# Kernel optimization log

Hardware: AMD Instinct MI355X
Metric: run time of the kernel (lower is better)

The kernel has to match this reference:

```python
import jax, jax.numpy as jnp
import numpy as np

B, U, C, M = 4096, 1024, 5000, 20

def setup_inputs() -> dict:
    key = jax.random.key(0)
    ks = jax.random.split(key, 9)
    inputs = jax.random.randint(ks[0], (B, 1), 0, C).astype(jnp.int32)
    states = 0.1 * jax.random.normal(ks[1], (B, U + 2), dtype=jnp.float32)
    bias_z = jnp.zeros((U,), jnp.float32)
    recurrent_kernel = 0.02 * jax.random.normal(ks[2], (U, 4 * U), dtype=jnp.float32)
    kernel_c = 0.02 * jax.random.normal(ks[3], (C, 4 * U), dtype=jnp.float32)
    bias = jnp.zeros((3 * U,), jnp.float32)
    kernel_d = 0.1 * jax.random.normal(ks[4], (2, 4 * U), dtype=jnp.float32)
    Wgmm_part1 = 0.05 * jax.random.normal(ks[5], (U, 3 * M), dtype=jnp.float32)
    bgmm_part1 = jnp.zeros((3 * M,), jnp.float32)
    return {"inputs": inputs, "states": states, "bias_z": bias_z,
            "recurrent_kernel": recurrent_kernel, "kernel_c": kernel_c,
            "bias": bias, "kernel_d": kernel_d,
            "Wgmm_part1": Wgmm_part1, "bgmm_part1": bgmm_part1}

def exp_safe(x):
    return jnp.clip(jnp.exp(x), 1e-10, 1e10)

def reference(inputs, states, bias_z, recurrent_kernel, kernel_c, bias,
              kernel_d, Wgmm_part1, bgmm_part1):
    u = bias_z.shape[0]
    h_tm1 = states[:, :-2]          # [B, U]
    _d = states[:, -2:]             # [B, 2]
    ch = inputs[:, 0].astype(jnp.int32)
    # one_hot(ch) @ kernel_c is just a row gather
    pre = kernel_c[ch] + _d @ kernel_d              # [B, 4U]
    # z and r gates share the left operand -> fuse into one matmul
    zr = (h_tm1 @ recurrent_kernel[:, :2 * u] + pre[:, :2 * u]
          + jnp.concatenate([bias_z, bias[:u]]))
    z = jax.nn.sigmoid(zr[:, :u])
    r = jax.nn.sigmoid(zr[:, u:])
    hh = jnp.tanh((r * h_tm1) @ recurrent_kernel[:, 2 * u:3 * u]
                  + pre[:, 2 * u:3 * u] + bias[u:2 * u])
    h = z * h_tm1 + (1.0 - z) * hh
    o = jnp.tanh(h @ recurrent_kernel[:, 3 * u:]
                 + pre[:, 3 * u:] + bias[2 * u:])
    gmm = o @ Wgmm_part1 + bgmm_part1               # [B, 3M]
    _pi, mux, muy = jnp.split(gmm, 3, axis=-1)
    e = exp_safe(_pi)
    pi = e / jnp.sum(e, axis=-1, keepdims=True)
    x_pred = jnp.sum(pi * mux, axis=-1, keepdims=True)
    y_pred = jnp.sum(pi * muy, axis=-1, keepdims=True)
    out = jnp.concatenate([o, pi, mux, muy, x_pred, y_pred], axis=-1)
    new_state = jnp.concatenate([h, x_pred, y_pred], axis=-1)
    return out, new_state
```

## Files before the change

### kernel.cpp

```cpp
#include <hip/hip_runtime.h>

typedef __attribute__((ext_vector_type(8))) short     bf16x8;
typedef __attribute__((ext_vector_type(4))) float     f32x4;
typedef __attribute__((ext_vector_type(2))) float     f32x2;
typedef __attribute__((ext_vector_type(4))) unsigned short u16x4;

#define NB 4096
#define NU 1024
#define OUT_STRIDE 1086
#define NS_STRIDE 1026
#define NS_BASE (4096*1086)

__device__ __forceinline__ unsigned short f2bf(float x) {
  unsigned int u = __float_as_uint(x);
  unsigned int r = (u + 0x7FFFu + ((u >> 16) & 1u)) >> 16;
  return (unsigned short)r;
}
__device__ __forceinline__ float sigmoidf(float x) { return 1.f / (1.f + expf(-x)); }

__device__ __forceinline__ void gld_lds16(const void* g, void* l) {
  __builtin_amdgcn_global_load_lds((const __attribute__((address_space(1))) void*)g,
                                   (__attribute__((address_space(3))) void*)l, 16, 0, 0);
}

__global__ __launch_bounds__(256)
void transposeR(const float* __restrict__ R, unsigned short* __restrict__ Bt) {
  __shared__ float t[64][65];
  const int tx = threadIdx.x & 63, ty = threadIdx.x >> 6;
  const int j0 = blockIdx.x * 64, k0 = blockIdx.y * 64;
#pragma unroll
  for (int i = 0; i < 64; i += 4)
    t[ty + i][tx] = R[(size_t)(k0 + ty + i) * 4096 + j0 + tx];
  __syncthreads();
#pragma unroll
  for (int i = 0; i < 64; i += 4) {
    const int j = ty + i;
    Bt[(size_t)(j0 + j) * 1024 + k0 + tx] = f2bf(t[tx][j]);
  }
}

__global__ __launch_bounds__(256)
void convertH(const float* __restrict__ states, unsigned short* __restrict__ hb) {
  const int idx = blockIdx.x * 256 + threadIdx.x;
  const int b = idx >> 8, u = (idx & 255) * 4;
  const float* sp = states + (size_t)b * 1026 + u;
  f32x2 v0 = *(const f32x2*)sp, v1 = *(const f32x2*)(sp + 2);
  u16x4 w;
  w[0] = f2bf(v0[0]); w[1] = f2bf(v0[1]); w[2] = f2bf(v1[0]); w[3] = f2bf(v1[1]);
  *(u16x4*)&hb[(size_t)b * 1024 + u] = w;
}

template<int EPI>
__global__ __launch_bounds__(256)
void gemm_k(const unsigned short* __restrict__ A,
            const unsigned short* __restrict__ Bt,
            float* __restrict__ C, int ldc,
            const int* __restrict__ chv,
            const float* __restrict__ states,
            const float* __restrict__ kc, int colbase,
            const float* __restrict__ kd,
            const float* __restrict__ bias, int biasoff,
            const float* __restrict__ zbuf,
            float* __restrict__ out2,
            unsigned short* __restrict__ hb2) {
  __shared__ unsigned short Al[128 * 32];
  __shared__ unsigned short Bl[128 * 32];
  __shared__ int   chs[128];
  __shared__ float d0s[128], d1s[128];

  const int tid = threadIdx.x;
  const int lane = tid & 63;
  const int wave = tid >> 6;
  const int wr = wave >> 1, wc = wave & 1;
  const int m0 = blockIdx.y * 128;
  const int n0 = blockIdx.x * 128;

  if (EPI != 0 && tid < 128) {
    const int r = m0 + tid;
    chs[tid] = chv[r];
    d0s[tid] = states[(size_t)r * 1026 + 1024];
    d1s[tid] = states[(size_t)r * 1026 + 1025];
  }

  f32x4 acc[4][4] = {};

  const int c0 = tid, c1 = tid + 256;
  const int ar0 = c0 >> 2, ak0 = (c0 & 3) * 8;
  const int ar1 = c1 >> 2, ak1 = (c1 & 3) * 8;
  const unsigned short* Ag = A + (size_t)m0 * 1024;
  const unsigned short* Bg = Bt + (size_t)n0 * 1024;

  for (int k0 = 0; k0 < 1024; k0 += 32) {
    __syncthreads();
    gld_lds16(Ag + (size_t)ar0 * 1024 + k0 + ak0, &Al[c0 * 8]);
    gld_lds16(Ag + (size_t)ar1 * 1024 + k0 + ak1, &Al[c1 * 8]);
    gld_lds16(Bg + (size_t)ar0 * 1024 + k0 + ak0, &Bl[c0 * 8]);
    gld_lds16(Bg + (size_t)ar1 * 1024 + k0 + ak1, &Bl[c1 * 8]);
    __syncthreads();
    bf16x8 af[4], bfr[4];
    const int arow = lane & 15, kg = (lane >> 4) * 8;
#pragma unroll
    for (int mi = 0; mi < 4; ++mi)
      af[mi] = *(const bf16x8*)&Al[(wr * 64 + mi * 16 + arow) * 32 + kg];
#pragma unroll
    for (int ni = 0; ni < 4; ++ni)
      bfr[ni] = *(const bf16x8*)&Bl[(wc * 64 + ni * 16 + arow) * 32 + kg];
#pragma unroll
    for (int mi = 0; mi < 4; ++mi)
#pragma unroll
      for (int ni = 0; ni < 4; ++ni)
        acc[mi][ni] = __builtin_amdgcn_mfma_f32_16x16x32_bf16(af[mi], bfr[ni], acc[mi][ni], 0, 0, 0);
  }

#pragma unroll
  for (int mi = 0; mi < 4; ++mi) {
#pragma unroll
    for (int r = 0; r < 4; ++r) {
      const int lrow = wr * 64 + mi * 16 + (lane >> 4) * 4 + r;
      const int grow = m0 + lrow;
      if (EPI == 0) {
#pragma unroll
        for (int ni = 0; ni < 4; ++ni) {
          const int gcol = n0 + wc * 64 + ni * 16 + (lane & 15);
          C[(size_t)grow * ldc + gcol] = acc[mi][ni][r];
        }
      } else {
        const int ch = chs[lrow];
        const float d0 = d0s[lrow], d1 = d1s[lrow];
        const float* kcrow = kc + (size_t)ch * 4096 + colbase;
#pragma unroll
        for (int ni = 0; ni < 4; ++ni) {
          const int gcol = n0 + wc * 64 + ni * 16 + (lane & 15);
          float v = acc[mi][ni][r] + kcrow[gcol]
                  + d0 * kd[colbase + gcol] + d1 * kd[4096 + colbase + gcol]
                  + bias[biasoff + gcol];
          if (EPI == 2) {
            const float hh = tanhf(v);
            const float z = zbuf[(size_t)grow * 1024 + gcol];
            const float htm = states[(size_t)grow * 1026 + gcol];
            const float h = z * htm + (1.f - z) * hh;
            out2[(size_t)grow * NS_STRIDE + gcol] = h;
            hb2[(size_t)grow * 1024 + gcol] = f2bf(h);
          } else {
            out2[(size_t)grow * OUT_STRIDE + gcol] = tanhf(v);
          }
        }
      }
    }
  }
}

__global__ __launch_bounds__(256)
void epi1_kernel(const float* __restrict__ zr,
                 const int* __restrict__ chv,
                 const float* __restrict__ states,
                 const float* __restrict__ kc,
                 const float* __restrict__ kd,
                 const float* __restrict__ bias_z,
                 const float* __restrict__ bias,
                 float* __restrict__ zbuf,
                 unsigned short* __restrict__ rh) {
  const int idx = blockIdx.x * 256 + threadIdx.x;
  const int b = idx >> 8, u = (idx & 255) * 4;
  const int ch = chv[b];
  const float* srow = states + (size_t)b * 1026;
  const float d0 = srow[1024], d1 = srow[1025];
  f32x4 az = *(const f32x4*)&zr[(size_t)b * 2048 + u];
  f32x4 ar = *(const f32x4*)&zr[(size_t)b * 2048 + 1024 + u];
  const float* kcrow = kc + (size_t)ch * 4096;
  f32x4 kz = *(const f32x4*)&kcrow[u];
  f32x4 kr = *(const f32x4*)&kcrow[1024 + u];
  f32x4 kd0z = *(const f32x4*)&kd[u];
  f32x4 kd1z = *(const f32x4*)&kd[4096 + u];
  f32x4 kd0r = *(const f32x4*)&kd[1024 + u];
  f32x4 kd1r = *(const f32x4*)&kd[4096 + 1024 + u];
  f32x4 bz = *(const f32x4*)&bias_z[u];
  f32x4 br = *(const f32x4*)&bias[u];
  f32x2 h01 = *(const f32x2*)&srow[u];
  f32x2 h23 = *(const f32x2*)&srow[u + 2];
  float hv[4] = {h01[0], h01[1], h23[0], h23[1]};
  f32x4 zout;
  u16x4 rhv;
#pragma unroll
  for (int i = 0; i < 4; ++i) {
    const float zi = sigmoidf(az[i] + kz[i] + d0 * kd0z[i] + d1 * kd1z[i] + bz[i]);
    const float ri = sigmoidf(ar[i] + kr[i] + d0 * kd0r[i] + d1 * kd1r[i] + br[i]);
    zout[i] = zi;
    rhv[i] = f2bf(ri * hv[i]);
  }
  *(f32x4*)&zbuf[(size_t)b * 1024 + u] = zout;
  *(u16x4*)&rh[(size_t)b * 1024 + u] = rhv;
}

__global__ __launch_bounds__(512)
void gmm_kernel(const float* __restrict__ obuf,
                const float* __restrict__ Wg,
                const float* __restrict__ bg,
                float* __restrict__ outp,
                float* __restrict__ ns) {
  __shared__ float Wl[128 * 60 + 16];
  __shared__ float ol[8 * 1024];
  const int tid = threadIdx.x;
  const int lane = tid & 63;
  const int wave = tid >> 6;
  const int row0 = blockIdx.x * 8;

  for (int i = tid; i < 4096; i += 512) {
    const int rr = i >> 9, c2 = (i & 511) * 2;
    *(f32x2*)&ol[rr * 1024 + c2] = *(const f32x2*)&obuf[(size_t)(row0 + rr) * OUT_STRIDE + c2];
  }

  float g = 0.f;
  for (int kc0 = 0; kc0 < 1024; kc0 += 128) {
    __syncthreads();
    for (int i = tid; i < 1920; i += 512)
      *(f32x4*)&Wl[i * 4] = *(const f32x4*)&Wg[kc0 * 60 + i * 4];
    __syncthreads();
    const float* orow = &ol[wave * 1024 + kc0];
#pragma unroll 8
    for (int k = 0; k < 128; ++k)
      g = fmaf(orow[k], Wl[k * 60 + lane], g);
  }
  if (lane < 60) g += bg[lane];

  float e = 0.f;
  if (lane < 20) e = fminf(fmaxf(expf(g), 1e-10f), 1e10f);
  float s = e;
#pragma unroll
  for (int m = 1; m < 32; m <<= 1) s += __shfl_xor(s, m, 64);
  const float pi = (lane < 20) ? e / s : 0.f;
  const int src1 = (lane < 20) ? lane + 20 : lane;
  const int src2 = (lane < 20) ? lane + 40 : lane;
  const float mux = __shfl(g, src1, 64);
  const float muy = __shfl(g, src2, 64);
  float px = pi * mux, py = pi * muy;
#pragma unroll
  for (int m = 1; m < 32; m <<= 1) { px += __shfl_xor(px, m, 64); py += __shfl_xor(py, m, 64); }

  const int row = row0 + wave;
  float* orow = outp + (size_t)row * OUT_STRIDE;
  if (lane < 20) orow[1024 + lane] = pi;
  else if (lane < 60) orow[1024 + lane] = g;
  if (lane == 0) {
    orow[1084] = px;
    orow[1085] = py;
    ns[(size_t)row * NS_STRIDE + 1024] = px;
    ns[(size_t)row * NS_STRIDE + 1025] = py;
  }
}

extern "C" void kernel_launch(void* const* d_in, const int* in_sizes, int n_in,
                              void* d_out, int out_size, void* d_ws, size_t ws_size,
                              hipStream_t stream) {
  const int*   chv     = (const int*)d_in[0];
  const float* states  = (const float*)d_in[1];
  const float* bias_z  = (const float*)d_in[2];
  const float* R       = (const float*)d_in[3];
  const float* kc      = (const float*)d_in[4];
  const float* bias    = (const float*)d_in[5];
  const float* kd      = (const float*)d_in[6];
  const float* Wg      = (const float*)d_in[7];
  const float* bg      = (const float*)d_in[8];
  float* out = (float*)d_out;

  char* ws = (char*)d_ws;
  unsigned short* RbT = (unsigned short*)ws;
  unsigned short* hb  = (unsigned short*)(ws + 8388608);
  float*          zr  = (float*)(ws + 16777216);
  float*          zbuf= (float*)(ws + 50331648);
  unsigned short* rh  = hb;
  unsigned short* hb2 = (unsigned short*)zr;

  transposeR<<<dim3(64, 16), 256, 0, stream>>>(R, RbT);
  convertH<<<4096, 256, 0, stream>>>(states, hb);

  gemm_k<0><<<dim3(16, 32), 256, 0, stream>>>(hb, RbT, zr, 2048,
      nullptr, nullptr, nullptr, 0, nullptr, nullptr, 0, nullptr, nullptr, nullptr);

  epi1_kernel<<<4096, 256, 0, stream>>>(zr, chv, states, kc, kd, bias_z, bias, zbuf, rh);

  gemm_k<2><<<dim3(8, 32), 256, 0, stream>>>(rh, RbT + (size_t)2048 * 1024, nullptr, 0,
      chv, states, kc, 2048, kd, bias, 1024, zbuf, out + NS_BASE, hb2);

  gemm_k<3><<<dim3(8, 32), 256, 0, stream>>>(hb2, RbT + (size_t)3072 * 1024, nullptr, 0,
      chv, states, kc, 3072, kd, bias, 2048, nullptr, out, nullptr);

  gmm_kernel<<<512, 512, 0, stream>>>(out, Wg, bg, out, out + NS_BASE);
}
```

Before: 343.9 us.

## Pipeline GEMM K-loop with 4-stage LDS ring, swizzle, XCD tile mapping, fuse gate epilogue

Rewrites the bf16 GEMM kernel to use a 4-buffer LDS ring with asynchronous global-to-LDS loads issued two stages ahead. Each step waits with vmcnt and a single barrier instead of two syncthreads per K step. LDS rows are XOR-swizzled to avoid bank conflicts, and block indices are remapped so neighbouring tiles share an XCD. The z/r sigmoid epilogue is fused into the first GEMM, which removes the separate epi1 kernel and the fp32 zr round trip through memory. The cost is more LDS per block (64KB plus extras) and tricky wait-count correctness.

New measurement: 357.0 us. +3.8%, slower.

```diff
diff --git a/kernel.cpp b/kernel.cpp
--- a/kernel.cpp
+++ b/kernel.cpp
@@ -5,8 +5,6 @@
 typedef __attribute__((ext_vector_type(2))) float     f32x2;
 typedef __attribute__((ext_vector_type(4))) unsigned short u16x4;
 
-#define NB 4096
-#define NU 1024
 #define OUT_STRIDE 1086
 #define NS_STRIDE 1026
 #define NS_BASE (4096*1086)
@@ -15,6 +13,9 @@
   unsigned int u = __float_as_uint(x);
   unsigned int r = (u + 0x7FFFu + ((u >> 16) & 1u)) >> 16;
   return (unsigned short)r;
+}
+__device__ __forceinline__ float bf2f(unsigned short u) {
+  union { unsigned int i; float f; } v; v.i = ((unsigned int)u) << 16; return v.f;
 }
 __device__ __forceinline__ float sigmoidf(float x) { return 1.f / (1.f + expf(-x)); }
 
@@ -50,146 +51,150 @@
   *(u16x4*)&hb[(size_t)b * 1024 + u] = w;
 }
 
-template<int EPI>
-__global__ __launch_bounds__(256)
-void gemm_k(const unsigned short* __restrict__ A,
-            const unsigned short* __restrict__ Bt,
-            float* __restrict__ C, int ldc,
-            const int* __restrict__ chv,
-            const float* __restrict__ states,
-            const float* __restrict__ kc, int colbase,
-            const float* __restrict__ kd,
-            const float* __restrict__ bias, int biasoff,
-            const float* __restrict__ zbuf,
-            float* __restrict__ out2,
-            unsigned short* __restrict__ hb2) {
-  __shared__ unsigned short Al[128 * 32];
-  __shared__ unsigned short Bl[128 * 32];
+template<int EPI, int NTN>
+__global__ __launch_bounds__(256, 2)
+void gemm_bt(const unsigned short* __restrict__ A,
+             const unsigned short* __restrict__ Bt, int colbase,
+             const int* __restrict__ chv,
+             const float* __restrict__ states,
+             const float* __restrict__ kcm,
+             const float* __restrict__ kd,
+             const float* __restrict__ bias_z,
+             const float* __restrict__ bias,
+             float* __restrict__ zbuf,
+             unsigned short* __restrict__ rh,
+             float* __restrict__ outp,
+             unsigned short* __restrict__ hb2) {
+  __shared__ __align__(16) char ldsb[65536];
   __shared__ int   chs[128];
   __shared__ float d0s[128], d1s[128];
 
-  const int tid = threadIdx.x;
-  const int lane = tid & 63;
-  const int wave = tid >> 6;
+  const int tid = threadIdx.x, lane = tid & 63, wave = tid >> 6;
   const int wr = wave >> 1, wc = wave & 1;
-  const int m0 = blockIdx.y * 128;
-  const int n0 = blockIdx.x * 128;
-
-  if (EPI != 0 && tid < 128) {
+  const int arow = lane & 15, q = lane >> 4;
+  const int bid = blockIdx.x;
+
+  int mt, nt;
+  if (NTN == 16) {
+    const int swz = (bid & 7) * 64 + (bid >> 3);
+    const int chunk = swz >> 6, l = swz & 63;
+    mt = (chunk & 3) * 8 + (l >> 3);
+    nt = (chunk >> 2) * 8 + (l & 7);
+  } else {
+    const int xcd = bid & 7, j = bid >> 3;
+    mt = xcd * 4 + (j >> 3);
+    nt = j & 7;
+  }
+  const int m0 = mt * 128, n0 = nt * 128;
+
+  if (tid < 128) {
     const int r = m0 + tid;
     chs[tid] = chv[r];
     d0s[tid] = states[(size_t)r * 1026 + 1024];
     d1s[tid] = states[(size_t)r * 1026 + 1025];
   }
 
+  const unsigned short* Ag = A  + (size_t)m0 * 1024;
+  const unsigned short* Bg = Bt + (size_t)(colbase + n0) * 1024;
+
   f32x4 acc[4][4] = {};
 
-  const int c0 = tid, c1 = tid + 256;
-  const int ar0 = c0 >> 2, ak0 = (c0 & 3) * 8;
-  const int ar1 = c1 >> 2, ak1 = (c1 & 3) * 8;
-  const unsigned short* Ag = A + (size_t)m0 * 1024;
-  const unsigned short* Bg = Bt + (size_t)n0 * 1024;
-
-  for (int k0 = 0; k0 < 1024; k0 += 32) {
-    __syncthreads();
-    gld_lds16(Ag + (size_t)ar0 * 1024 + k0 + ak0, &Al[c0 * 8]);
-    gld_lds16(Ag + (size_t)ar1 * 1024 + k0 + ak1, &Al[c1 * 8]);
-    gld_lds16(Bg + (size_t)ar0 * 1024 + k0 + ak0, &Bl[c0 * 8]);
-    gld_lds16(Bg + (size_t)ar1 * 1024 + k0 + ak1, &Bl[c1 * 8]);
-    __syncthreads();
+#define ST1(c, G, Loff, kk) {                                                  \
+    const int row_ = (c) >> 2;                                                 \
+    const int ss_  = ((c) & 3) ^ (row_ & 3);                                   \
+    gld_lds16(G + (size_t)row_ * 1024 + (kk) + ss_ * 8, ldsb + (Loff) + (c) * 16); }
+#define STAGE(b, kk) {                                                         \
+    ST1(tid,       Ag, (b) * 8192,         kk)                                 \
+    ST1(tid + 256, Ag, (b) * 8192,         kk)                                 \
+    ST1(tid,       Bg, 32768 + (b) * 8192, kk)                                 \
+    ST1(tid + 256, Bg, 32768 + (b) * 8192, kk) }
+
+  const int sq = (q ^ (arow & 3)) << 4;
+
+  auto compute = [&](int cb) {
     bf16x8 af[4], bfr[4];
-    const int arow = lane & 15, kg = (lane >> 4) * 8;
-#pragma unroll
-    for (int mi = 0; mi < 4; ++mi)
-      af[mi] = *(const bf16x8*)&Al[(wr * 64 + mi * 16 + arow) * 32 + kg];
-#pragma unroll
-    for (int ni = 0; ni < 4; ++ni)
-      bfr[ni] = *(const bf16x8*)&Bl[(wc * 64 + ni * 16 + arow) * 32 + kg];
+    const char* Ab = ldsb + cb * 8192;
+    const char* Bb = ldsb + 32768 + cb * 8192;
+#pragma unroll
+    for (int mi = 0; mi < 4; ++mi) {
+      const int R = wr * 64 + mi * 16 + arow;
+      af[mi] = *(const bf16x8*)(Ab + R * 64 + sq);
+    }
+#pragma unroll
+    for (int ni = 0; ni < 4; ++ni) {
+      const int R = wc * 64 + ni * 16 + arow;
+      bfr[ni] = *(const bf16x8*)(Bb + R * 64 + sq);
+    }
+    __builtin_amdgcn_s_setprio(1);
 #pragma unroll
     for (int mi = 0; mi < 4; ++mi)
 #pragma unroll
       for (int ni = 0; ni < 4; ++ni)
         acc[mi][ni] = __builtin_amdgcn_mfma_f32_16x16x32_bf16(af[mi], bfr[ni], acc[mi][ni], 0, 0, 0);
-  }
+    __builtin_amdgcn_s_setprio(0);
+  };
+
+  STAGE(0, 0)
+  STAGE(1, 32)
+  for (int t = 0; t < 30; ++t) {
+    STAGE((t + 2) & 3, (t + 2) * 32)
+    asm volatile("s_waitcnt vmcnt(8)" ::: "memory");
+    __builtin_amdgcn_s_barrier();
+    asm volatile("" ::: "memory");
+    compute(t & 3);
+  }
+  asm volatile("s_waitcnt vmcnt(4)" ::: "memory");
+  __builtin_amdgcn_s_barrier();
+  asm volatile("" ::: "memory");
+  compute(2);
+  asm volatile("s_waitcnt vmcnt(0)" ::: "memory");
+  __builtin_amdgcn_s_barrier();
+  asm volatile("" ::: "memory");
+  compute(3);
+#undef STAGE
+#undef ST1
 
 #pragma unroll
   for (int mi = 0; mi < 4; ++mi) {
 #pragma unroll
-    for (int r = 0; r < 4; ++r) {
-      const int lrow = wr * 64 + mi * 16 + (lane >> 4) * 4 + r;
+    for (int i = 0; i < 4; ++i) {
+      const int lrow = wr * 64 + mi * 16 + q * 4 + i;
       const int grow = m0 + lrow;
-      if (EPI == 0) {
-#pragma unroll
-        for (int ni = 0; ni < 4; ++ni) {
-          const int gcol = n0 + wc * 64 + ni * 16 + (lane & 15);
-          C[(size_t)grow * ldc + gcol] = acc[mi][ni][r];
-        }
-      } else {
-        const int ch = chs[lrow];
-        const float d0 = d0s[lrow], d1 = d1s[lrow];
-        const float* kcrow = kc + (size_t)ch * 4096 + colbase;
-#pragma unroll
-        for (int ni = 0; ni < 4; ++ni) {
-          const int gcol = n0 + wc * 64 + ni * 16 + (lane & 15);
-          float v = acc[mi][ni][r] + kcrow[gcol]
-                  + d0 * kd[colbase + gcol] + d1 * kd[4096 + colbase + gcol]
-                  + bias[biasoff + gcol];
-          if (EPI == 2) {
-            const float hh = tanhf(v);
-            const float z = zbuf[(size_t)grow * 1024 + gcol];
-            const float htm = states[(size_t)grow * 1026 + gcol];
-            const float h = z * htm + (1.f - z) * hh;
-            out2[(size_t)grow * NS_STRIDE + gcol] = h;
-            hb2[(size_t)grow * 1024 + gcol] = f2bf(h);
+      const int ch = chs[lrow];
+      const float d0 = d0s[lrow], d1 = d1s[lrow];
+      const float* kcr = kcm + (size_t)ch * 4096;
+#pragma unroll
+      for (int ni = 0; ni < 4; ++ni) {
+        const int gc = n0 + wc * 64 + ni * 16 + arow;
+        const float a = acc[mi][ni][i];
+        if (EPI == 1) {
+          const int fullc = gc;
+          const float pre = kcr[fullc] + d0 * kd[fullc] + d1 * kd[4096 + fullc];
+          if (n0 < 1024) {
+            const float z = sigmoidf(a + pre + bias_z[gc]);
+            zbuf[(size_t)grow * 1024 + gc] = z;
           } else {
-            out2[(size_t)grow * OUT_STRIDE + gcol] = tanhf(v);
+            const int uc = gc - 1024;
+            const float r = sigmoidf(a + pre + bias[uc]);
+            rh[(size_t)grow * 1024 + uc] = f2bf(r * states[(size_t)grow * 1026 + uc]);
           }
+        } else if (EPI == 2) {
+          const int fullc = 2048 + gc;
+          const float v = a + kcr[fullc] + d0 * kd[fullc] + d1 * kd[4096 + fullc] + bias[1024 + gc];
+          const float hh = tanhf(v);
+          const float z = zbuf[(size_t)grow * 1024 + gc];
+          const float htm = states[(size_t)grow * 1026 + gc];
+          const float h = z * htm + (1.f - z) * hh;
+          outp[(size_t)grow * NS_STRIDE + gc] = h;
+          hb2[(size_t)grow * 1024 + gc] = f2bf(h);
+        } else {
+          const int fullc = 3072 + gc;
+          const float v = a + kcr[fullc] + d0 * kd[fullc] + d1 * kd[4096 + fullc] + bias[2048 + gc];
+          outp[(size_t)grow * OUT_STRIDE + gc] = tanhf(v);
         }
       }
     }
   }
-}
-
-__global__ __launch_bounds__(256)
-void epi1_kernel(const float* __restrict__ zr,
-                 const int* __restrict__ chv,
-                 const float* __restrict__ states,
-                 const float* __restrict__ kc,
-                 const float* __restrict__ kd,
-                 const float* __restrict__ bias_z,
-                 const float* __restrict__ bias,
-                 float* __restrict__ zbuf,
-                 unsigned short* __restrict__ rh) {
-  const int idx = blockIdx.x * 256 + threadIdx.x;
-  const int b = idx >> 8, u = (idx & 255) * 4;
-  const int ch = chv[b];
-  const float* srow = states + (size_t)b * 1026;
-  const float d0 = srow[1024], d1 = srow[1025];
-  f32x4 az = *(const f32x4*)&zr[(size_t)b * 2048 + u];
-  f32x4 ar = *(const f32x4*)&zr[(size_t)b * 2048 + 1024 + u];
-  const float* kcrow = kc + (size_t)ch * 4096;
-  f32x4 kz = *(const f32x4*)&kcrow[u];
-  f32x4 kr = *(const f32x4*)&kcrow[1024 + u];
-  f32x4 kd0z = *(const f32x4*)&kd[u];
-  f32x4 kd1z = *(const f32x4*)&kd[4096 + u];
-  f32x4 kd0r = *(const f32x4*)&kd[1024 + u];
-  f32x4 kd1r = *(const f32x4*)&kd[4096 + 1024 + u];
-  f32x4 bz = *(const f32x4*)&bias_z[u];
-  f32x4 br = *(const f32x4*)&bias[u];
-  f32x2 h01 = *(const f32x2*)&srow[u];
-  f32x2 h23 = *(const f32x2*)&srow[u + 2];
-  float hv[4] = {h01[0], h01[1], h23[0], h23[1]};
-  f32x4 zout;
-  u16x4 rhv;
-#pragma unroll
-  for (int i = 0; i < 4; ++i) {
-    const float zi = sigmoidf(az[i] + kz[i] + d0 * kd0z[i] + d1 * kd1z[i] + bz[i]);
-    const float ri = sigmoidf(ar[i] + kr[i] + d0 * kd0r[i] + d1 * kd1r[i] + br[i]);
-    zout[i] = zi;
-    rhv[i] = f2bf(ri * hv[i]);
-  }
-  *(f32x4*)&zbuf[(size_t)b * 1024 + u] = zout;
-  *(u16x4*)&rh[(size_t)b * 1024 + u] = rhv;
 }
 
 __global__ __launch_bounds__(512)
@@ -252,38 +257,35 @@
 extern "C" void kernel_launch(void* const* d_in, const int* in_sizes, int n_in,
                               void* d_out, int out_size, void* d_ws, size_t ws_size,
                               hipStream_t stream) {
-  const int*   chv     = (const int*)d_in[0];
-  const float* states  = (const float*)d_in[1];
-  const float* bias_z  = (const float*)d_in[2];
-  const float* R       = (const float*)d_in[3];
-  const float* kc      = (const float*)d_in[4];
-  const float* bias    = (const float*)d_in[5];
-  const float* kd      = (const float*)d_in[6];
-  const float* Wg      = (const float*)d_in[7];
-  const float* bg      = (const float*)d_in[8];
+  const int*   chv    = (const int*)d_in[0];
+  const float* states = (const float*)d_in[1];
+  const float* bias_z = (const float*)d_in[2];
+  const float* R      = (const float*)d_in[3];
+  const float* kc     = (const float*)d_in[4];
+  const float* bias   = (const float*)d_in[5];
+  const float* kd     = (const float*)d_in[6];
+  const float* Wg     = (const float*)d_in[7];
+  const float* bg     = (const float*)d_in[8];
   float* out = (float*)d_out;
 
   char* ws = (char*)d_ws;
-  unsigned short* RbT = (unsigned short*)ws;
-  unsigned short* hb  = (unsigned short*)(ws + 8388608);
-  float*          zr  = (float*)(ws + 16777216);
-  float*          zbuf= (float*)(ws + 50331648);
-  unsigned short* rh  = hb;
-  unsigned short* hb2 = (unsigned short*)zr;
+  unsigned short* RbT  = (unsigned short*)ws;
+  unsigned short* hb   = (unsigned short*)(ws + 8388608);
+  unsigned short* rh   = (unsigned short*)(ws + 16777216);
+  unsigned short* hb2  = (unsigned short*)(ws + 25165824);
+  float*          zbuf = (float*)(ws + 33554432);
 
   transposeR<<<dim3(64, 16), 256, 0, stream>>>(R, RbT);
   convertH<<<4096, 256, 0, stream>>>(states, hb);
 
-  gemm_k<0><<<dim3(16, 32), 256, 0, stream>>>(hb, RbT, zr, 2048,
-      nullptr, nullptr, nullptr, 0, nullptr, nullptr, 0, nullptr, nullptr, nullptr);
-
-  epi1_kernel<<<4096, 256, 0, stream>>>(zr, chv, states, kc, kd, bias_z, bias, zbuf, rh);
-
-  gemm_k<2><<<dim3(8, 32), 256, 0, stream>>>(rh, RbT + (size_t)2048 * 1024, nullptr, 0,
-      chv, states, kc, 2048, kd, bias, 1024, zbuf, out + NS_BASE, hb2);
-
-  gemm_k<3><<<dim3(8, 32), 256, 0, stream>>>(hb2, RbT + (size_t)3072 * 1024, nullptr, 0,
-      chv, states, kc, 3072, kd, bias, 2048, nullptr, out, nullptr);
+  gemm_bt<1, 16><<<512, 256, 0, stream>>>(hb, RbT, 0,
+      chv, states, kc, kd, bias_z, bias, zbuf, rh, nullptr, nullptr);
+
+  gemm_bt<2, 8><<<256, 256, 0, stream>>>(rh, RbT, 2048,
+      chv, states, kc, kd, bias_z, bias, zbuf, nullptr, out + NS_BASE, hb2);
+
+  gemm_bt<3, 8><<<256, 256, 0, stream>>>(hb2, RbT, 3072,
+      chv, states, kc, kd, bias_z, bias, nullptr, nullptr, out, nullptr);
 
   gmm_kernel<<<512, 512, 0, stream>>>(out, Wg, bg, out, out + NS_BASE);
 }
```
